# Optimization experiments

Measured on AMD Instinct MI355X. Metric: run time of the kernel, lower is better.

The kernel has to match this reference:

```python
import jax, jax.numpy as jnp
import numpy as np

Q_NUM, K_DIM, Q_DIM, F_DIM = 4, 10, 10, 10


def conv2d(x, w, b=None):
    # x: (B,Cin,H,W), w: (Cout,Cin,kh,kw), VALID padding, stride 1
    y = jax.lax.conv_general_dilated(x, w, (1, 1), 'VALID',
                                     dimension_numbers=('NCHW', 'OIHW', 'NCHW'))
    if b is not None:
        y = y + b[None, :, None, None]
    return y


def add_coords(x):
    # xx varies along H (dim 2), yy along W (dim 3); both normalized to [-1, 1]
    B, _, H, W = x.shape
    xx = jnp.broadcast_to(jnp.linspace(-1.0, 1.0, H, dtype=x.dtype)[None, None, :, None], (B, 1, H, W))
    yy = jnp.broadcast_to(jnp.linspace(-1.0, 1.0, W, dtype=x.dtype)[None, None, None, :], (B, 1, H, W))
    return jnp.concatenate([x, xx, yy], axis=1)


def positional_encodings(H, W, dtype=jnp.float32):
    # (H*W, 2): x in [0,1] along width, y in [0,1] along height
    x_lin = jnp.broadcast_to(jnp.linspace(0.0, 1.0, W, dtype=dtype)[None, :], (H, W))
    y_lin = jnp.broadcast_to(jnp.linspace(0.0, 1.0, H, dtype=dtype)[:, None], (H, W))
    return jnp.stack([x_lin.reshape(-1), y_lin.reshape(-1)], axis=-1)


def setup_inputs() -> dict:
    key = jax.random.key(0)
    ks = jax.random.split(key, 10)
    CH = K_DIM * Q_NUM  # 40

    def he(k, shape, fan_in):
        return jax.random.normal(k, shape, dtype=jnp.float32) * np.float32(np.sqrt(2.0 / fan_in))

    return {
        'in_img': jax.random.normal(ks[0], (64, 3, 128, 128), dtype=jnp.float32),
        'w1': he(ks[1], (16, 5, 3, 3), 5 * 9),
        'b1': jnp.zeros((16,), jnp.float32),
        'w2': he(ks[2], (32, 16, 3, 3), 16 * 9),
        'b2': jnp.zeros((32,), jnp.float32),
        'w3': he(ks[3], (CH, 32, 3, 3), 32 * 9),
        'b3': jnp.zeros((CH,), jnp.float32),
        'k_w': he(ks[4], (CH, CH, 1, 1), CH),
        'f_w': he(ks[5], (CH, CH, 1, 1), CH),
        'query': jax.random.normal(ks[6], (Q_NUM, Q_DIM), dtype=jnp.float32) * np.float32(np.sqrt(2.0 / Q_NUM)),
    }


def reference(in_img, w1, b1, w2, b2, w3, b3, k_w, f_w, query):
    x = add_coords(in_img)
    x = jax.nn.relu(conv2d(x, w1, b1))
    x = jax.nn.relu(conv2d(x, w2, b2))
    x = jax.nn.relu(conv2d(x, w3, b3))  # (B, 40, H', W')
    B, _, H, W = x.shape

    # key: (B,H,W,K_DIM,Q_NUM) after NCHW->NHWC permute and channel split (c = d*Q_NUM + q)
    k = conv2d(x, k_w).transpose(0, 2, 3, 1).reshape(B, H, W, K_DIM, Q_NUM)

    # Original computes query@key (B,H,W,Q,Q), masks with eye, sums -> diagonal only.
    # Equivalent: direct per-query dot products.
    scale = jnp.sqrt(jnp.asarray(H * W, dtype=x.dtype))
    scores = jnp.einsum('qd,bhwdq->bhwq', query, k) / scale  # (B,H,W,Q)
    logits = scores.transpose(0, 3, 1, 2).reshape(B, Q_NUM, H * W)
    att_map = jax.nn.softmax(logits, axis=-1)[:, :, None, :]  # (B,Q,1,HW)

    pt = positional_encodings(H, W, x.dtype)  # (HW, 2)
    pt_value = jnp.broadcast_to(pt[None, None], (B, Q_NUM, H * W, 2))

    fv = conv2d(x, f_w).reshape(B, F_DIM, Q_NUM, H * W).transpose(0, 2, 3, 1)  # (B,Q,HW,F)

    pt_out = jnp.matmul(att_map, pt_value).reshape(B, Q_NUM * 2)
    feat_out = jnp.matmul(att_map, fv).reshape(B, F_DIM * Q_NUM)
    return (x, pt_out, feat_out, att_map)
```

## Files before the change

kernel.cpp:

```cpp
#include <hip/hip_runtime.h>
#include <hip/hip_bf16.h>

constexpr int BATCH = 64;
constexpr int H1 = 126, W1 = 126, C1 = 16;
constexpr int H2 = 124, W2 = 124, C2 = 32;
constexpr int H3 = 122, W3 = 122, C3 = 40;
constexpr int HW3 = H3 * W3;

typedef __attribute__((ext_vector_type(8))) short bf16x8;
typedef __attribute__((ext_vector_type(4))) float f32x4;

__device__ __forceinline__ ushort f2bf(float f) {
    __hip_bfloat16 h = __float2bfloat16(f);
    return *reinterpret_cast<ushort*>(&h);
}

constexpr size_t IMGN_B  = 0;
constexpr size_t IMGN_SZ = (size_t)BATCH * 128 * 128 * 8 * 2;
constexpr size_t A1_B    = (IMGN_B + IMGN_SZ + 255) & ~(size_t)255;
constexpr size_t A1_SZB  = (size_t)BATCH * H1 * W1 * C1 * 2;
constexpr size_t A2_B    = (A1_B + A1_SZB + 255) & ~(size_t)255;
constexpr size_t A2_SZB  = (size_t)BATCH * H2 * W2 * C2 * 2;
constexpr size_t BT1_B   = (A2_B + A2_SZB + 255) & ~(size_t)255;
constexpr size_t BT2_B   = (BT1_B + 16 * 96 * 2 + 255) & ~(size_t)255;
constexpr size_t BT3_B   = (BT2_B + 32 * 160 * 2 + 255) & ~(size_t)255;
constexpr size_t QKW_B   = (BT3_B + 48 * 288 * 2 + 255) & ~(size_t)255;
constexpr size_t SMAT_B  = (QKW_B + 160 * 4 + 255) & ~(size_t)255;

constexpr size_t X_SZ     = (size_t)BATCH * C3 * HW3;
constexpr size_t PT_OFF   = X_SZ;
constexpr size_t FEAT_OFF = PT_OFF + BATCH * 8;
constexpr size_t ATT_OFF  = FEAT_OFF + BATCH * 40;

__global__ void k_qkw(const float* __restrict__ query, const float* __restrict__ k_w,
                      float* __restrict__ qkw) {
    int t = threadIdx.x;
    if (t < 160) {
        int q = t / 40, c = t % 40;
        float s = 0.f;
        #pragma unroll
        for (int d = 0; d < 10; ++d)
            s = fmaf(query[q * 10 + d], k_w[(d * 4 + q) * 40 + c], s);
        qkw[t] = s * (1.0f / 122.0f);
    }
}

__global__ void k_bt(const float* __restrict__ w1, ushort* __restrict__ bt1,
                     const float* __restrict__ w2, ushort* __restrict__ bt2,
                     const float* __restrict__ w3, ushort* __restrict__ bt3) {
    int t = blockIdx.x * 256 + threadIdx.x;
    if (t < 16 * 96) {
        int oc = t / 96, k = t % 96, cell = k >> 3, c = k & 7;
        float v = (c < 5 && cell < 9) ? w1[(oc * 5 + c) * 9 + cell] : 0.f;
        bt1[t] = f2bf(v);
    } else if (t < 16 * 96 + 32 * 160) {
        int u = t - 16 * 96;
        int n = u / 160, k = u % 160;
        float v = 0.f;
        if (k < 144) { int c = k & 15, cell = k >> 4; v = w2[(n * 16 + c) * 9 + cell]; }
        bt2[u] = f2bf(v);
    } else {
        int u = t - 16 * 96 - 32 * 160;
        if (u < 48 * 288) {
            int n = u / 288, k = u % 288;
            float v = 0.f;
            if (n < 40) { int c = k & 31, cell = k >> 5; v = w3[(n * 32 + c) * 9 + cell]; }
            bt3[u] = f2bf(v);
        }
    }
}

__global__ __launch_bounds__(256) void k_imgN(const float* __restrict__ img,
                                              ushort* __restrict__ imgN) {
    int tid = blockIdx.x * 256 + threadIdx.x;
    int b = tid >> 14, pix = tid & 16383;
    int y = pix >> 7, xc = pix & 127;
    const float* ip = img + (size_t)b * 3 * 16384 + pix;
    bf16x8 v;
    v[0] = (short)f2bf(ip[0]);
    v[1] = (short)f2bf(ip[16384]);
    v[2] = (short)f2bf(ip[32768]);
    v[3] = (short)f2bf(-1.0f + (2.0f / 127.0f) * (float)y);
    v[4] = (short)f2bf(-1.0f + (2.0f / 127.0f) * (float)xc);
    v[5] = 0; v[6] = 0; v[7] = 0;
    *(bf16x8*)(imgN + (size_t)tid * 8) = v;
}

__global__ __launch_bounds__(256) void k_conv1_mfma(const ushort* __restrict__ imgN,
                                                    const ushort* __restrict__ bt1,
                                                    const float* __restrict__ b1,
                                                    ushort* __restrict__ a1) {
    __shared__ ushort sx1[256][16];
    const int b = blockIdx.y, y0 = blockIdx.x * 2;
    const int t = threadIdx.x, lane = t & 63, w = t >> 6;
    const int col = lane & 15, g = lane >> 4;
    const int ro = w >> 1, xbase = (w & 1) * 64;

    f32x4 acc[4];
    const float bv = b1[col];
    #pragma unroll
    for (int mi = 0; mi < 4; ++mi) acc[mi] = (f32x4){bv, bv, bv, bv};

    #pragma unroll
    for (int ks = 0; ks < 3; ++ks) {
        bf16x8 bf = *(const bf16x8*)(bt1 + (size_t)col * 96 + ks * 32 + 8 * g);
        const int cell = ks * 4 + g;
        const bool valid = (cell < 9);
        const int ky = cell / 3, kx = cell % 3;
        #pragma unroll
        for (int mi = 0; mi < 4; ++mi) {
            const int xcol = xbase + mi * 16 + col;
            bf16x8 af = (bf16x8)0;
            if (valid) {
                const int row = y0 + ro + ky;
                const int xin = min(xcol + kx, 127);
                af = *(const bf16x8*)(imgN + (((size_t)b * 128 + row) * 128 + xin) * 8);
            }
            acc[mi] = __builtin_amdgcn_mfma_f32_16x16x32_bf16(af, bf, acc[mi], 0, 0, 0);
        }
    }

    #pragma unroll
    for (int mi = 0; mi < 4; ++mi) {
        const int m0 = w * 64 + mi * 16 + 4 * g;
        #pragma unroll
        for (int r = 0; r < 4; ++r)
            sx1[m0 + r][col] = f2bf(fmaxf(acc[mi][r], 0.0f));
    }
    __syncthreads();

    ushort* op = a1 + ((size_t)b * H1 + y0) * W1 * C1;
    for (int i = t; i < 504; i += 256) {
        int ro2 = i / 252, r = i % 252, xcol = r >> 1, c0 = (r & 1) * 8;
        *(bf16x8*)(op + ((size_t)ro2 * W1 + xcol) * C1 + c0) =
            *(const bf16x8*)(&sx1[ro2 * 128 + xcol][c0]);
    }
}

__global__ __launch_bounds__(256) void k_conv2_mfma(const ushort* __restrict__ a1,
                                                    const ushort* __restrict__ bt2,
                                                    const float* __restrict__ b2,
                                                    ushort* __restrict__ a2) {
    __shared__ ushort sx2[256][40];
    const int b = blockIdx.y, y0 = blockIdx.x * 2;
    const int t = threadIdx.x, lane = t & 63, w = t >> 6;
    const int col = lane & 15, g = lane >> 4;
    const int ro = w >> 1, xbase = (w & 1) * 64;

    f32x4 acc[4][2];
    #pragma unroll
    for (int mi = 0; mi < 4; ++mi)
        #pragma unroll
        for (int nf = 0; nf < 2; ++nf) {
            float bv = b2[nf * 16 + col];
            acc[mi][nf] = (f32x4){bv, bv, bv, bv};
        }

    #pragma unroll
    for (int ks = 0; ks < 5; ++ks) {
        bf16x8 bf[2];
        #pragma unroll
        for (int nf = 0; nf < 2; ++nf)
            bf[nf] = *(const bf16x8*)(bt2 + (size_t)(nf * 16 + col) * 160 + ks * 32 + 8 * g);
        const int cell = 2 * ks + (g >> 1);
        const bool valid = (cell <= 8);
        const int ky = cell / 3, kx = cell - ky * 3;
        const int c0 = 8 * (g & 1);
        #pragma unroll
        for (int mi = 0; mi < 4; ++mi) {
            const int xcol = xbase + mi * 16 + col;
            bf16x8 af = (bf16x8)0;
            if (valid) {
                const int row = y0 + ro + ky;
                const int xin = min(xcol + kx, W1 - 1);
                af = *(const bf16x8*)(a1 + (((size_t)b * H1 + row) * W1 + xin) * C1 + c0);
            }
            #pragma unroll
            for (int nf = 0; nf < 2; ++nf)
                acc[mi][nf] = __builtin_amdgcn_mfma_f32_16x16x32_bf16(af, bf[nf], acc[mi][nf], 0, 0, 0);
        }
    }

    #pragma unroll
    for (int mi = 0; mi < 4; ++mi) {
        const int m0 = w * 64 + mi * 16 + 4 * g;
        #pragma unroll
        for (int nf = 0; nf < 2; ++nf)
            #pragma unroll
            for (int r = 0; r < 4; ++r)
                sx2[m0 + r][nf * 16 + col] = f2bf(fmaxf(acc[mi][nf][r], 0.0f));
    }
    __syncthreads();

    ushort* op = a2 + ((size_t)b * H2 + y0) * W2 * C2;
    for (int i = t; i < 992; i += 256) {
        int ro2 = i / 496, r = i % 496, xcol = r >> 2, c0 = (r & 3) * 8;
        *(bf16x8*)(op + ((size_t)ro2 * W2 + xcol) * C2 + c0) =
            *(const bf16x8*)(&sx2[ro2 * 128 + xcol][c0]);
    }
}

__global__ __launch_bounds__(256) void k_conv3_mfma(const ushort* __restrict__ a2,
                                                    const ushort* __restrict__ bt3,
                                                    const float* __restrict__ b3,
                                                    const float* __restrict__ qkw,
                                                    float* __restrict__ x,
                                                    float* __restrict__ att) {
    __shared__ float sx[256][41];
    __shared__ float lq[160];
    const int b = blockIdx.y, y0 = blockIdx.x * 2;
    const int t = threadIdx.x, lane = t & 63, w = t >> 6;
    const int col = lane & 15, g = lane >> 4;
    const int ro = w >> 1, xbase = (w & 1) * 64;

    f32x4 acc[4][3];
    #pragma unroll
    for (int mi = 0; mi < 4; ++mi)
        #pragma unroll
        for (int nf = 0; nf < 3; ++nf) {
            const int ch = nf * 16 + col;
            float bv = (ch < 40) ? b3[ch] : 0.f;
            acc[mi][nf] = (f32x4){bv, bv, bv, bv};
        }

    #pragma unroll
    for (int ky = 0; ky < 3; ++ky) {
        #pragma unroll
        for (int kx = 0; kx < 3; ++kx) {
            const int ks = ky * 3 + kx;
            bf16x8 bf[3];
            #pragma unroll
            for (int nf = 0; nf < 3; ++nf)
                bf[nf] = *(const bf16x8*)(bt3 + (size_t)(nf * 16 + col) * 288 + ks * 32 + 8 * g);
            const ushort* arow = a2 + ((size_t)b * H2 + (y0 + ro + ky)) * W2 * C2;
            #pragma unroll
            for (int mi = 0; mi < 4; ++mi) {
                const int xcol = xbase + mi * 16 + col;
                const int xin = min(xcol + kx, W2 - 1);
                bf16x8 af = *(const bf16x8*)(arow + (size_t)xin * C2 + 8 * g);
                #pragma unroll
                for (int nf = 0; nf < 3; ++nf)
                    acc[mi][nf] = __builtin_amdgcn_mfma_f32_16x16x32_bf16(af, bf[nf], acc[mi][nf], 0, 0, 0);
            }
        }
    }

    for (int i = t; i < 160; i += 256) lq[i] = qkw[i];
    #pragma unroll
    for (int mi = 0; mi < 4; ++mi) {
        const int m0 = w * 64 + mi * 16 + 4 * g;
        #pragma unroll
        for (int nf = 0; nf < 3; ++nf) {
            const int ch = nf * 16 + col;
            if (ch < 40) {
                #pragma unroll
                for (int r = 0; r < 4; ++r)
                    sx[m0 + r][ch] = fmaxf(acc[mi][nf][r], 0.0f);
            }
        }
    }
    __syncthreads();

    if (t < 244) {
        const int ro2 = (t >= 122) ? 1 : 0;
        const int xcol = t - ro2 * 122;
        const int srow = ro2 * 128 + xcol;
        const int p = (y0 + ro2) * W3 + xcol;
        float* xp = x + (size_t)b * C3 * HW3 + p;
        float s0 = 0, s1 = 0, s2 = 0, s3 = 0;
        #pragma unroll
        for (int c = 0; c < 40; ++c) {
            float v = sx[srow][c];
            xp[(size_t)c * HW3] = v;
            s0 = fmaf(v, lq[c], s0);
            s1 = fmaf(v, lq[40 + c], s1);
            s2 = fmaf(v, lq[80 + c], s2);
            s3 = fmaf(v, lq[120 + c], s3);
        }
        float* ap = att + (size_t)b * 4 * HW3 + p;
        ap[0] = s0; ap[HW3] = s1; ap[2 * HW3] = s2; ap[3 * HW3] = s3;
    }
}

__device__ __forceinline__ float block_max(float v, float* sred) {
    #pragma unroll
    for (int off = 32; off >= 1; off >>= 1) v = fmaxf(v, __shfl_xor(v, off));
    if ((threadIdx.x & 63) == 0) sred[threadIdx.x >> 6] = v;
    __syncthreads();
    float r = fmaxf(fmaxf(sred[0], sred[1]), fmaxf(sred[2], sred[3]));
    __syncthreads();
    return r;
}
__device__ __forceinline__ float block_sum(float v, float* sred) {
    #pragma unroll
    for (int off = 32; off >= 1; off >>= 1) v += __shfl_xor(v, off);
    if ((threadIdx.x & 63) == 0) sred[threadIdx.x >> 6] = v;
    __syncthreads();
    float r = sred[0] + sred[1] + sred[2] + sred[3];
    __syncthreads();
    return r;
}

__global__ __launch_bounds__(256) void k_softmax(float* __restrict__ att,
                                                 float* __restrict__ pt_out) {
    __shared__ float sred[4];
    const int bq = blockIdx.x;
    float* row = att + (size_t)bq * HW3;
    const int t = threadIdx.x;

    float m_t = -1e30f, s_t = 0.f;
    for (int p = t; p < HW3; p += 256) {
        float v = row[p];
        if (v <= m_t) {
            s_t += __expf(v - m_t);
        } else {
            s_t = s_t * __expf(m_t - v) + 1.0f;
            m_t = v;
        }
    }
    float M = block_max(m_t, sred);
    s_t *= __expf(m_t - M);
    float S = block_sum(s_t, sred);
    const float inv = 1.0f / S;

    float sx = 0.f, sy = 0.f;
    for (int p = t; p < HW3; p += 256) {
        float wgt = __expf(row[p] - M) * inv;
        row[p] = wgt;
        int pr = p / W3, pc = p % W3;
        sx = fmaf(wgt, (float)pc * (1.0f / (W3 - 1)), sx);
        sy = fmaf(wgt, (float)pr * (1.0f / (H3 - 1)), sy);
    }
    sx = block_sum(sx, sred);
    sy = block_sum(sy, sred);
    if (t == 0) { pt_out[bq * 2] = sx; pt_out[bq * 2 + 1] = sy; }
}

__global__ __launch_bounds__(256) void k_smat(const float* __restrict__ x,
                                              const float* __restrict__ att,
                                              float* __restrict__ smat) {
    __shared__ float sred[4];
    const int c = blockIdx.x, b = blockIdx.y;
    const float* xp = x + ((size_t)b * C3 + c) * HW3;
    const float* ap = att + (size_t)b * 4 * HW3;
    float a0 = 0, a1 = 0, a2 = 0, a3 = 0;
    for (int p = threadIdx.x; p < HW3; p += 256) {
        float v = xp[p];
        a0 = fmaf(v, ap[p], a0);
        a1 = fmaf(v, ap[HW3 + p], a1);
        a2 = fmaf(v, ap[2 * HW3 + p], a2);
        a3 = fmaf(v, ap[3 * HW3 + p], a3);
    }
    a0 = block_sum(a0, sred);
    a1 = block_sum(a1, sred);
    a2 = block_sum(a2, sred);
    a3 = block_sum(a3, sred);
    if (threadIdx.x == 0) {
        smat[((size_t)b * 4 + 0) * 40 + c] = a0;
        smat[((size_t)b * 4 + 1) * 40 + c] = a1;
        smat[((size_t)b * 4 + 2) * 40 + c] = a2;
        smat[((size_t)b * 4 + 3) * 40 + c] = a3;
    }
}

__global__ void k_feat(const float* __restrict__ smat, const float* __restrict__ f_w,
                       float* __restrict__ feat) {
    const int b = blockIdx.x, t = threadIdx.x;
    if (t < 40) {
        int q = t / 10, d = t % 10;
        float s = 0.f;
        #pragma unroll
        for (int c = 0; c < 40; ++c)
            s = fmaf(f_w[(d * 4 + q) * 40 + c], smat[((size_t)b * 4 + q) * 40 + c], s);
        feat[b * 40 + t] = s;
    }
}

extern "C" void kernel_launch(void* const* d_in, const int* in_sizes, int n_in,
                              void* d_out, int out_size, void* d_ws, size_t ws_size,
                              hipStream_t stream) {
    const float* img   = (const float*)d_in[0];
    const float* w1    = (const float*)d_in[1];
    const float* b1    = (const float*)d_in[2];
    const float* w2    = (const float*)d_in[3];
    const float* b2    = (const float*)d_in[4];
    const float* w3    = (const float*)d_in[5];
    const float* b3    = (const float*)d_in[6];
    const float* k_w   = (const float*)d_in[7];
    const float* f_w   = (const float*)d_in[8];
    const float* query = (const float*)d_in[9];

    char* ws = (char*)d_ws;
    ushort* imgN = (ushort*)(ws + IMGN_B);
    ushort* a1   = (ushort*)(ws + A1_B);
    ushort* a2   = (ushort*)(ws + A2_B);
    ushort* bt1  = (ushort*)(ws + BT1_B);
    ushort* bt2  = (ushort*)(ws + BT2_B);
    ushort* bt3  = (ushort*)(ws + BT3_B);
    float*  qkw  = (float*)(ws + QKW_B);
    float*  smat = (float*)(ws + SMAT_B);

    float* out  = (float*)d_out;
    float* x    = out;
    float* pt   = out + PT_OFF;
    float* feat = out + FEAT_OFF;
    float* att  = out + ATT_OFF;

    k_qkw<<<1, 256, 0, stream>>>(query, k_w, qkw);
    k_bt<<<80, 256, 0, stream>>>(w1, bt1, w2, bt2, w3, bt3);
    k_imgN<<<(BATCH * 16384) / 256, 256, 0, stream>>>(img, imgN);
    k_conv1_mfma<<<dim3(63, BATCH), 256, 0, stream>>>(imgN, bt1, b1, a1);
    k_conv2_mfma<<<dim3(62, BATCH), 256, 0, stream>>>(a1, bt2, b2, a2);
    k_conv3_mfma<<<dim3(61, BATCH), 256, 0, stream>>>(a2, bt3, b3, qkw, x, att);
    k_softmax<<<BATCH * 4, 256, 0, stream>>>(att, pt);
    k_smat<<<dim3(40, BATCH), 256, 0, stream>>>(x, att, smat);
    k_feat<<<BATCH, 64, 0, stream>>>(smat, f_w, feat);
}
```

Measured before the change: 416.1 us.

## Store conv3 output from registers, stage bf16 in LDS, chunk smat reduction with atomics

The conv3 kernel now writes the fp32 activation tensor straight from MFMA accumulators with paired-float stores, instead of staging fp32 in shared memory and writing per channel. Only a bf16 copy is kept in shared memory to compute the attention logits, which shrinks LDS use but rounds the inputs to the query-key dot products. The smat reduction is split into pixel chunks per batch, with all 40 channels in one block and partial sums combined by atomicAdd into a zeroed buffer, so attention rows are reused across channels. The cost is less coalesced scattered stores in conv3, a small numerical change in the logits, and non-deterministic summation order.

```diff
diff --git a/kernel.cpp b/kernel.cpp
--- a/kernel.cpp
+++ b/kernel.cpp
@@ -9,10 +9,14 @@
 
 typedef __attribute__((ext_vector_type(8))) short bf16x8;
 typedef __attribute__((ext_vector_type(4))) float f32x4;
+typedef __attribute__((ext_vector_type(2))) float f32x2;
 
 __device__ __forceinline__ ushort f2bf(float f) {
     __hip_bfloat16 h = __float2bfloat16(f);
     return *reinterpret_cast<ushort*>(&h);
+}
+__device__ __forceinline__ float bf2f(ushort u) {
+    return __uint_as_float((unsigned)u << 16);
 }
 
 constexpr size_t IMGN_B  = 0;
@@ -206,7 +210,7 @@
                                                     const float* __restrict__ qkw,
                                                     float* __restrict__ x,
                                                     float* __restrict__ att) {
-    __shared__ float sx[256][41];
+    __shared__ ushort sxb[256][44];
     __shared__ float lq[160];
     const int b = blockIdx.y, y0 = blockIdx.x * 2;
     const int t = threadIdx.x, lane = t & 63, w = t >> 6;
@@ -246,16 +250,29 @@
     }
 
     for (int i = t; i < 160; i += 256) lq[i] = qkw[i];
+
     #pragma unroll
     for (int mi = 0; mi < 4; ++mi) {
         const int m0 = w * 64 + mi * 16 + 4 * g;
+        const int ro2 = m0 >> 7, xc0 = m0 & 127;
+        const int row = y0 + ro2;
         #pragma unroll
         for (int nf = 0; nf < 3; ++nf) {
             const int ch = nf * 16 + col;
             if (ch < 40) {
+                f32x4 v;
                 #pragma unroll
-                for (int r = 0; r < 4; ++r)
-                    sx[m0 + r][ch] = fmaxf(acc[mi][nf][r], 0.0f);
+                for (int r = 0; r < 4; ++r) v[r] = fmaxf(acc[mi][nf][r], 0.0f);
+                #pragma unroll
+                for (int r = 0; r < 4; ++r) sxb[m0 + r][ch] = f2bf(v[r]);
+                if (xc0 < 120) {
+                    float* xp = x + ((size_t)b * C3 + ch) * HW3 + (size_t)row * W3 + xc0;
+                    *(f32x2*)xp       = (f32x2){v[0], v[1]};
+                    *(f32x2*)(xp + 2) = (f32x2){v[2], v[3]};
+                } else if (xc0 == 120) {
+                    float* xp = x + ((size_t)b * C3 + ch) * HW3 + (size_t)row * W3 + xc0;
+                    *(f32x2*)xp = (f32x2){v[0], v[1]};
+                }
             }
         }
     }
@@ -265,18 +282,22 @@
         const int ro2 = (t >= 122) ? 1 : 0;
         const int xcol = t - ro2 * 122;
         const int srow = ro2 * 128 + xcol;
+        const ushort* rowp = &sxb[srow][0];
+        float s0 = 0, s1 = 0, s2 = 0, s3 = 0;
+        #pragma unroll
+        for (int k = 0; k < 10; ++k) {
+            uint2 u = *(const uint2*)(rowp + 4 * k);
+            float v0 = bf2f((ushort)(u.x & 0xffff));
+            float v1 = bf2f((ushort)(u.x >> 16));
+            float v2 = bf2f((ushort)(u.y & 0xffff));
+            float v3 = bf2f((ushort)(u.y >> 16));
+            const int c = 4 * k;
+            s0 = fmaf(v0, lq[c], fmaf(v1, lq[c + 1], fmaf(v2, lq[c + 2], fmaf(v3, lq[c + 3], s0))));
+            s1 = fmaf(v0, lq[40 + c], fmaf(v1, lq[41 + c], fmaf(v2, lq[42 + c], fmaf(v3, lq[43 + c], s1))));
+            s2 = fmaf(v0, lq[80 + c], fmaf(v1, lq[81 + c], fmaf(v2, lq[82 + c], fmaf(v3, lq[83 + c], s2))));
+            s3 = fmaf(v0, lq[120 + c], fmaf(v1, lq[121 + c], fmaf(v2, lq[122 + c], fmaf(v3, lq[123 + c], s3))));
+        }
         const int p = (y0 + ro2) * W3 + xcol;
-        float* xp = x + (size_t)b * C3 * HW3 + p;
-        float s0 = 0, s1 = 0, s2 = 0, s3 = 0;
-        #pragma unroll
-        for (int c = 0; c < 40; ++c) {
-            float v = sx[srow][c];
-            xp[(size_t)c * HW3] = v;
-            s0 = fmaf(v, lq[c], s0);
-            s1 = fmaf(v, lq[40 + c], s1);
-            s2 = fmaf(v, lq[80 + c], s2);
-            s3 = fmaf(v, lq[120 + c], s3);
-        }
         float* ap = att + (size_t)b * 4 * HW3 + p;
         ap[0] = s0; ap[HW3] = s1; ap[2 * HW3] = s2; ap[3 * HW3] = s3;
     }
@@ -336,30 +357,38 @@
     if (t == 0) { pt_out[bq * 2] = sx; pt_out[bq * 2 + 1] = sy; }
 }
 
-__global__ __launch_bounds__(256) void k_smat(const float* __restrict__ x,
+constexpr int SM_CHUNKS = 16;
+constexpr int SM_CHUNK  = (HW3 + SM_CHUNKS - 1) / SM_CHUNKS;
+__global__ __launch_bounds__(320) void k_smat(const float* __restrict__ x,
                                               const float* __restrict__ att,
                                               float* __restrict__ smat) {
-    __shared__ float sred[4];
-    const int c = blockIdx.x, b = blockIdx.y;
+    const int chunk = blockIdx.x, b = blockIdx.y;
+    const int t = threadIdx.x;
+    const int c = t >> 3, pl = t & 7;
+    const int p0 = chunk * SM_CHUNK;
+    const int pend = min(p0 + SM_CHUNK, HW3);
     const float* xp = x + ((size_t)b * C3 + c) * HW3;
     const float* ap = att + (size_t)b * 4 * HW3;
     float a0 = 0, a1 = 0, a2 = 0, a3 = 0;
-    for (int p = threadIdx.x; p < HW3; p += 256) {
+    for (int p = p0 + pl; p < pend; p += 8) {
         float v = xp[p];
         a0 = fmaf(v, ap[p], a0);
         a1 = fmaf(v, ap[HW3 + p], a1);
         a2 = fmaf(v, ap[2 * HW3 + p], a2);
         a3 = fmaf(v, ap[3 * HW3 + p], a3);
     }
-    a0 = block_sum(a0, sred);
-    a1 = block_sum(a1, sred);
-    a2 = block_sum(a2, sred);
-    a3 = block_sum(a3, sred);
-    if (threadIdx.x == 0) {
-        smat[((size_t)b * 4 + 0) * 40 + c] = a0;
-        smat[((size_t)b * 4 + 1) * 40 + c] = a1;
-        smat[((size_t)b * 4 + 2) * 40 + c] = a2;
-        smat[((size_t)b * 4 + 3) * 40 + c] = a3;
+    #pragma unroll
+    for (int off = 4; off >= 1; off >>= 1) {
+        a0 += __shfl_xor(a0, off);
+        a1 += __shfl_xor(a1, off);
+        a2 += __shfl_xor(a2, off);
+        a3 += __shfl_xor(a3, off);
+    }
+    if (pl == 0) {
+        atomicAdd(&smat[((size_t)b * 4 + 0) * 40 + c], a0);
+        atomicAdd(&smat[((size_t)b * 4 + 1) * 40 + c], a1);
+        atomicAdd(&smat[((size_t)b * 4 + 2) * 40 + c], a2);
+        atomicAdd(&smat[((size_t)b * 4 + 3) * 40 + c], a3);
     }
 }
 
@@ -406,6 +435,7 @@
     float* feat = out + FEAT_OFF;
     float* att  = out + ATT_OFF;
 
+    hipMemsetAsync(smat, 0, (size_t)BATCH * 4 * 40 * sizeof(float), stream);
     k_qkw<<<1, 256, 0, stream>>>(query, k_w, qkw);
     k_bt<<<80, 256, 0, stream>>>(w1, bt1, w2, bt2, w3, bt3);
     k_imgN<<<(BATCH * 16384) / 256, 256, 0, stream>>>(img, imgN);
@@ -413,6 +443,6 @@
     k_conv2_mfma<<<dim3(62, BATCH), 256, 0, stream>>>(a1, bt2, b2, a2);
     k_conv3_mfma<<<dim3(61, BATCH), 256, 0, stream>>>(a2, bt3, b3, qkw, x, att);
     k_softmax<<<BATCH * 4, 256, 0, stream>>>(att, pt);
-    k_smat<<<dim3(40, BATCH), 256, 0, stream>>>(x, att, smat);
+    k_smat<<<dim3(SM_CHUNKS, BATCH), 320, 0, stream>>>(x, att, smat);
     k_feat<<<BATCH, 64, 0, stream>>>(smat, f_w, feat);
 }
```

Measured after the change: 434.2 us. 1.04x slower.

## Fuse softmax and attention-weighted reductions into conv3 epilogue with atomics

Applied to the files above, without the earlier changes.

The conv3 epilogue now computes exp(logits) directly, without subtracting a max, and writes them out. It accumulates per-block partial sums of the softmax denominator, the position-weighted sums and the channel-by-attention sums, then adds them into workspace with atomics. A small finish kernel normalizes pt and feat, and a separate pass rescales the attention map. This removes the standalone softmax and smat kernels, which reread the full x and att tensors from memory. It also stages x in bf16 shared memory and writes it back with coalesced paired stores. The trade-offs are that the x output is now rounded to bf16, exp can overflow when logits are large, and the float atomics make the reductions nondeterministic.

```diff
diff --git a/kernel.cpp b/kernel.cpp
--- a/kernel.cpp
+++ b/kernel.cpp
@@ -9,10 +9,14 @@
 
 typedef __attribute__((ext_vector_type(8))) short bf16x8;
 typedef __attribute__((ext_vector_type(4))) float f32x4;
+typedef __attribute__((ext_vector_type(2))) float f32x2;
 
 __device__ __forceinline__ ushort f2bf(float f) {
     __hip_bfloat16 h = __float2bfloat16(f);
     return *reinterpret_cast<ushort*>(&h);
+}
+__device__ __forceinline__ float bf2f(ushort u) {
+    return __uint_as_float((unsigned)u << 16);
 }
 
 constexpr size_t IMGN_B  = 0;
@@ -25,7 +29,11 @@
 constexpr size_t BT2_B   = (BT1_B + 16 * 96 * 2 + 255) & ~(size_t)255;
 constexpr size_t BT3_B   = (BT2_B + 32 * 160 * 2 + 255) & ~(size_t)255;
 constexpr size_t QKW_B   = (BT3_B + 48 * 288 * 2 + 255) & ~(size_t)255;
-constexpr size_t SMAT_B  = (QKW_B + 160 * 4 + 255) & ~(size_t)255;
+constexpr size_t SMATR_B = (QKW_B + 160 * 4 + 255) & ~(size_t)255;
+constexpr size_t SR_B    = SMATR_B + (size_t)BATCH * 160 * 4;
+constexpr size_t PTR_B   = SR_B + (size_t)BATCH * 4 * 4;
+constexpr size_t RAW_SZB = (size_t)BATCH * 160 * 4 + (size_t)BATCH * 4 * 4 + (size_t)BATCH * 8 * 4;
+constexpr size_t INV_B   = (SMATR_B + RAW_SZB + 255) & ~(size_t)255;
 
 constexpr size_t X_SZ     = (size_t)BATCH * C3 * HW3;
 constexpr size_t PT_OFF   = X_SZ;
@@ -205,9 +213,15 @@
                                                     const float* __restrict__ b3,
                                                     const float* __restrict__ qkw,
                                                     float* __restrict__ x,
-                                                    float* __restrict__ att) {
-    __shared__ float sx[256][41];
+                                                    float* __restrict__ att,
+                                                    float* __restrict__ smat_raw,
+                                                    float* __restrict__ S_raw,
+                                                    float* __restrict__ pt_raw) {
+    __shared__ ushort sxb[256][42];
+    __shared__ f32x4 se4[244];
+    __shared__ float ls[6][4][40];
     __shared__ float lq[160];
+    __shared__ float sr12[4][12];
     const int b = blockIdx.y, y0 = blockIdx.x * 2;
     const int t = threadIdx.x, lane = t & 63, w = t >> 6;
     const int col = lane & 15, g = lane >> 4;
@@ -255,124 +269,138 @@
             if (ch < 40) {
                 #pragma unroll
                 for (int r = 0; r < 4; ++r)
-                    sx[m0 + r][ch] = fmaxf(acc[mi][nf][r], 0.0f);
+                    sxb[m0 + r][ch] = f2bf(fmaxf(acc[mi][nf][r], 0.0f));
             }
         }
     }
     __syncthreads();
 
+    float e0 = 0, e1 = 0, e2 = 0, e3 = 0, pxv = 0, pyv = 0;
     if (t < 244) {
         const int ro2 = (t >= 122) ? 1 : 0;
         const int xcol = t - ro2 * 122;
         const int srow = ro2 * 128 + xcol;
+        const ushort* rowp = &sxb[srow][0];
+        float s0 = 0, s1 = 0, s2 = 0, s3 = 0;
+        #pragma unroll
+        for (int k = 0; k < 10; ++k) {
+            uint ua = *(const uint*)(rowp + 4 * k);
+            uint ub = *(const uint*)(rowp + 4 * k + 2);
+            float v0 = bf2f((ushort)(ua & 0xffff));
+            float v1 = bf2f((ushort)(ua >> 16));
+            float v2 = bf2f((ushort)(ub & 0xffff));
+            float v3 = bf2f((ushort)(ub >> 16));
+            const int c = 4 * k;
+            s0 = fmaf(v0, lq[c], fmaf(v1, lq[c + 1], fmaf(v2, lq[c + 2], fmaf(v3, lq[c + 3], s0))));
+            s1 = fmaf(v0, lq[40 + c], fmaf(v1, lq[41 + c], fmaf(v2, lq[42 + c], fmaf(v3, lq[43 + c], s1))));
+            s2 = fmaf(v0, lq[80 + c], fmaf(v1, lq[81 + c], fmaf(v2, lq[82 + c], fmaf(v3, lq[83 + c], s2))));
+            s3 = fmaf(v0, lq[120 + c], fmaf(v1, lq[121 + c], fmaf(v2, lq[122 + c], fmaf(v3, lq[123 + c], s3))));
+        }
+        e0 = __expf(s0); e1 = __expf(s1); e2 = __expf(s2); e3 = __expf(s3);
         const int p = (y0 + ro2) * W3 + xcol;
-        float* xp = x + (size_t)b * C3 * HW3 + p;
-        float s0 = 0, s1 = 0, s2 = 0, s3 = 0;
-        #pragma unroll
-        for (int c = 0; c < 40; ++c) {
-            float v = sx[srow][c];
-            xp[(size_t)c * HW3] = v;
-            s0 = fmaf(v, lq[c], s0);
-            s1 = fmaf(v, lq[40 + c], s1);
-            s2 = fmaf(v, lq[80 + c], s2);
-            s3 = fmaf(v, lq[120 + c], s3);
-        }
         float* ap = att + (size_t)b * 4 * HW3 + p;
-        ap[0] = s0; ap[HW3] = s1; ap[2 * HW3] = s2; ap[3 * HW3] = s3;
-    }
-}
-
-__device__ __forceinline__ float block_max(float v, float* sred) {
-    #pragma unroll
-    for (int off = 32; off >= 1; off >>= 1) v = fmaxf(v, __shfl_xor(v, off));
-    if ((threadIdx.x & 63) == 0) sred[threadIdx.x >> 6] = v;
-    __syncthreads();
-    float r = fmaxf(fmaxf(sred[0], sred[1]), fmaxf(sred[2], sred[3]));
-    __syncthreads();
-    return r;
-}
-__device__ __forceinline__ float block_sum(float v, float* sred) {
-    #pragma unroll
-    for (int off = 32; off >= 1; off >>= 1) v += __shfl_xor(v, off);
-    if ((threadIdx.x & 63) == 0) sred[threadIdx.x >> 6] = v;
-    __syncthreads();
-    float r = sred[0] + sred[1] + sred[2] + sred[3];
-    __syncthreads();
-    return r;
-}
-
-__global__ __launch_bounds__(256) void k_softmax(float* __restrict__ att,
-                                                 float* __restrict__ pt_out) {
-    __shared__ float sred[4];
-    const int bq = blockIdx.x;
-    float* row = att + (size_t)bq * HW3;
-    const int t = threadIdx.x;
-
-    float m_t = -1e30f, s_t = 0.f;
-    for (int p = t; p < HW3; p += 256) {
-        float v = row[p];
-        if (v <= m_t) {
-            s_t += __expf(v - m_t);
-        } else {
-            s_t = s_t * __expf(m_t - v) + 1.0f;
-            m_t = v;
-        }
-    }
-    float M = block_max(m_t, sred);
-    s_t *= __expf(m_t - M);
-    float S = block_sum(s_t, sred);
-    const float inv = 1.0f / S;
-
-    float sx = 0.f, sy = 0.f;
-    for (int p = t; p < HW3; p += 256) {
-        float wgt = __expf(row[p] - M) * inv;
-        row[p] = wgt;
-        int pr = p / W3, pc = p % W3;
-        sx = fmaf(wgt, (float)pc * (1.0f / (W3 - 1)), sx);
-        sy = fmaf(wgt, (float)pr * (1.0f / (H3 - 1)), sy);
-    }
-    sx = block_sum(sx, sred);
-    sy = block_sum(sy, sred);
-    if (t == 0) { pt_out[bq * 2] = sx; pt_out[bq * 2 + 1] = sy; }
-}
-
-__global__ __launch_bounds__(256) void k_smat(const float* __restrict__ x,
-                                              const float* __restrict__ att,
-                                              float* __restrict__ smat) {
-    __shared__ float sred[4];
-    const int c = blockIdx.x, b = blockIdx.y;
-    const float* xp = x + ((size_t)b * C3 + c) * HW3;
-    const float* ap = att + (size_t)b * 4 * HW3;
-    float a0 = 0, a1 = 0, a2 = 0, a3 = 0;
-    for (int p = threadIdx.x; p < HW3; p += 256) {
-        float v = xp[p];
-        a0 = fmaf(v, ap[p], a0);
-        a1 = fmaf(v, ap[HW3 + p], a1);
-        a2 = fmaf(v, ap[2 * HW3 + p], a2);
-        a3 = fmaf(v, ap[3 * HW3 + p], a3);
-    }
-    a0 = block_sum(a0, sred);
-    a1 = block_sum(a1, sred);
-    a2 = block_sum(a2, sred);
-    a3 = block_sum(a3, sred);
-    if (threadIdx.x == 0) {
-        smat[((size_t)b * 4 + 0) * 40 + c] = a0;
-        smat[((size_t)b * 4 + 1) * 40 + c] = a1;
-        smat[((size_t)b * 4 + 2) * 40 + c] = a2;
-        smat[((size_t)b * 4 + 3) * 40 + c] = a3;
-    }
-}
-
-__global__ void k_feat(const float* __restrict__ smat, const float* __restrict__ f_w,
-                       float* __restrict__ feat) {
+        ap[0] = e0; ap[HW3] = e1; ap[2 * HW3] = e2; ap[3 * HW3] = e3;
+        se4[t] = (f32x4){e0, e1, e2, e3};
+        pxv = (float)xcol * (1.0f / 121.0f);
+        pyv = (float)(y0 + ro2) * (1.0f / 121.0f);
+    }
+    __syncthreads();
+
+    {
+        float v[12] = {e0, e1, e2, e3,
+                       e0 * pxv, e1 * pxv, e2 * pxv, e3 * pxv,
+                       e0 * pyv, e1 * pyv, e2 * pyv, e3 * pyv};
+        #pragma unroll
+        for (int off = 32; off >= 1; off >>= 1)
+            #pragma unroll
+            for (int k = 0; k < 12; ++k) v[k] += __shfl_xor(v[k], off);
+        if (lane == 0)
+            #pragma unroll
+            for (int k = 0; k < 12; ++k) sr12[w][k] = v[k];
+    }
+
+    if (t < 240) {
+        const int c = t % 40, j = t / 40;
+        float a0 = 0, a1 = 0, a2s = 0, a3 = 0;
+        for (int p = j; p < 244; p += 6) {
+            const int prow = p + ((p >= 122) ? 6 : 0);
+            float xv = bf2f(sxb[prow][c]);
+            f32x4 ev = se4[p];
+            a0 = fmaf(xv, ev[0], a0);
+            a1 = fmaf(xv, ev[1], a1);
+            a2s = fmaf(xv, ev[2], a2s);
+            a3 = fmaf(xv, ev[3], a3);
+        }
+        ls[j][0][c] = a0; ls[j][1][c] = a1; ls[j][2][c] = a2s; ls[j][3][c] = a3;
+    }
+
+    for (int i = t; i < 4880; i += 256) {
+        const int run = i / 61, pp = i % 61;
+        const int ro2 = run / 40, ch = run % 40;
+        const int pos = pp * 2;
+        const int srow = ro2 * 128 + pos;
+        float va = bf2f(sxb[srow][ch]);
+        float vb = bf2f(sxb[srow + 1][ch]);
+        float* xp = x + ((size_t)b * C3 + ch) * HW3 + (size_t)(y0 + ro2) * W3 + pos;
+        *(f32x2*)xp = (f32x2){va, vb};
+    }
+    __syncthreads();
+
+    if (t < 160) {
+        const int q = t / 40, c = t % 40;
+        float s = ls[0][q][c] + ls[1][q][c] + ls[2][q][c] +
+                  ls[3][q][c] + ls[4][q][c] + ls[5][q][c];
+        atomicAdd(&smat_raw[(size_t)b * 160 + q * 40 + c], s);
+    }
+    if (t == 0) {
+        #pragma unroll
+        for (int k = 0; k < 4; ++k) {
+            float sv = sr12[0][k] + sr12[1][k] + sr12[2][k] + sr12[3][k];
+            atomicAdd(&S_raw[b * 4 + k], sv);
+        }
+        #pragma unroll
+        for (int k = 0; k < 4; ++k) {
+            float sx = sr12[0][4 + k] + sr12[1][4 + k] + sr12[2][4 + k] + sr12[3][4 + k];
+            float sy = sr12[0][8 + k] + sr12[1][8 + k] + sr12[2][8 + k] + sr12[3][8 + k];
+            atomicAdd(&pt_raw[b * 8 + k * 2], sx);
+            atomicAdd(&pt_raw[b * 8 + k * 2 + 1], sy);
+        }
+    }
+}
+
+__global__ void k_finish(const float* __restrict__ S_raw, const float* __restrict__ pt_raw,
+                         const float* __restrict__ smat_raw, const float* __restrict__ f_w,
+                         float* __restrict__ pt_out, float* __restrict__ feat,
+                         float* __restrict__ invS) {
+    __shared__ float linv[4];
     const int b = blockIdx.x, t = threadIdx.x;
+    if (t < 4) {
+        float iv = 1.0f / S_raw[b * 4 + t];
+        linv[t] = iv;
+        invS[b * 4 + t] = iv;
+    }
+    __syncthreads();
     if (t < 40) {
-        int q = t / 10, d = t % 10;
+        const int q = t / 10, d = t % 10;
         float s = 0.f;
         #pragma unroll
         for (int c = 0; c < 40; ++c)
-            s = fmaf(f_w[(d * 4 + q) * 40 + c], smat[((size_t)b * 4 + q) * 40 + c], s);
-        feat[b * 40 + t] = s;
+            s = fmaf(f_w[(d * 4 + q) * 40 + c], smat_raw[(size_t)b * 160 + q * 40 + c], s);
+        feat[b * 40 + t] = s * linv[q];
+    }
+    if (t < 8) pt_out[b * 8 + t] = pt_raw[b * 8 + t] * linv[t >> 1];
+}
+
+__global__ __launch_bounds__(256) void k_attnorm(float* __restrict__ att,
+                                                 const float* __restrict__ invS) {
+    const int bq = blockIdx.y;
+    const float iv = invS[bq];
+    f32x4* a4 = (f32x4*)(att + (size_t)bq * HW3);
+    constexpr int N4 = HW3 / 4;
+    for (int i = blockIdx.x * 256 + threadIdx.x; i < N4; i += 4 * 256) {
+        f32x4 v = a4[i];
+        v[0] *= iv; v[1] *= iv; v[2] *= iv; v[3] *= iv;
+        a4[i] = v;
     }
 }
 
@@ -398,7 +426,10 @@
     ushort* bt2  = (ushort*)(ws + BT2_B);
     ushort* bt3  = (ushort*)(ws + BT3_B);
     float*  qkw  = (float*)(ws + QKW_B);
-    float*  smat = (float*)(ws + SMAT_B);
+    float*  smat_raw = (float*)(ws + SMATR_B);
+    float*  S_raw    = (float*)(ws + SR_B);
+    float*  pt_raw   = (float*)(ws + PTR_B);
+    float*  invS     = (float*)(ws + INV_B);
 
     float* out  = (float*)d_out;
     float* x    = out;
@@ -406,13 +437,14 @@
     float* feat = out + FEAT_OFF;
     float* att  = out + ATT_OFF;
 
+    hipMemsetAsync(smat_raw, 0, RAW_SZB, stream);
     k_qkw<<<1, 256, 0, stream>>>(query, k_w, qkw);
     k_bt<<<80, 256, 0, stream>>>(w1, bt1, w2, bt2, w3, bt3);
     k_imgN<<<(BATCH * 16384) / 256, 256, 0, stream>>>(img, imgN);
     k_conv1_mfma<<<dim3(63, BATCH), 256, 0, stream>>>(imgN, bt1, b1, a1);
     k_conv2_mfma<<<dim3(62, BATCH), 256, 0, stream>>>(a1, bt2, b2, a2);
-    k_conv3_mfma<<<dim3(61, BATCH), 256, 0, stream>>>(a2, bt3, b3, qkw, x, att);
-    k_softmax<<<BATCH * 4, 256, 0, stream>>>(att, pt);
-    k_smat<<<dim3(40, BATCH), 256, 0, stream>>>(x, att, smat);
-    k_feat<<<BATCH, 64, 0, stream>>>(smat, f_w, feat);
-}
+    k_conv3_mfma<<<dim3(61, BATCH), 256, 0, stream>>>(a2, bt3, b3, qkw, x, att,
+                                                      smat_raw, S_raw, pt_raw);
+    k_finish<<<BATCH, 64, 0, stream>>>(S_raw, pt_raw, smat_raw, f_w, pt, feat, invS);
+    k_attnorm<<<dim3(4, BATCH * 4), 256, 0, stream>>>(att, invS);
+}
```

New measurement: 412.5 us. Within noise of the previous version (-0.9%).
